# Performance work log

Hardware: AMD Instinct MI355X
Metric: run time of the kernel (lower is better)

## Reference

```python
import jax, jax.numpy as jnp
import numpy as np

INF = 1e5
EPS = 1e-8
B, NRES, NRIG = 1, 448, 512
C_S, C_Z, C_H, H, PQ, PV = 384, 128, 16, 12, 4, 8


def _quat_to_rot(q):
    q = q / jnp.linalg.norm(q, axis=-1, keepdims=True)
    w, x, y, z = q[..., 0], q[..., 1], q[..., 2], q[..., 3]
    return jnp.stack([
        jnp.stack([1 - 2 * (y * y + z * z), 2 * (x * y - w * z), 2 * (x * z + w * y)], -1),
        jnp.stack([2 * (x * y + w * z), 1 - 2 * (x * x + z * z), 2 * (y * z - w * x)], -1),
        jnp.stack([2 * (x * z - w * y), 2 * (y * z + w * x), 1 - 2 * (x * x + y * y)], -1),
    ], -2)


def setup_inputs() -> dict:
    key = jax.random.key(0)
    ks = jax.random.split(key, 16)
    lin = lambda k, i, o: (jax.random.normal(k, (i, o), jnp.float32) / np.sqrt(i))
    hc = H * C_H
    return dict(
        s=jax.random.normal(ks[0], (B, NRIG, C_S), jnp.float32),
        z=jax.random.normal(ks[1], (B, NRES, NRES, C_Z), jnp.float32),
        rot=_quat_to_rot(jax.random.normal(ks[2], (B, NRIG, 4), jnp.float32)),
        trans=jax.random.normal(ks[3], (B, NRIG, 3), jnp.float32) * 10.0,
        mask=jnp.ones((B, NRIG), jnp.float32),
        rigid_to_res_idx=jax.random.randint(ks[4], (B, NRIG), 0, NRES),
        w_q=lin(ks[5], C_S, hc), b_q=jnp.zeros((hc,), jnp.float32),
        w_kv=lin(ks[6], C_S, 2 * hc), b_kv=jnp.zeros((2 * hc,), jnp.float32),
        w_qp=lin(ks[7], C_S, H * PQ * 3), b_qp=jnp.zeros((H * PQ * 3,), jnp.float32),
        w_kvp=lin(ks[8], C_S, H * (PQ + PV) * 3), b_kvp=jnp.zeros((H * (PQ + PV) * 3,), jnp.float32),
        w_b=lin(ks[9], C_Z, H), b_b=jnp.zeros((H,), jnp.float32),
        w_dz=lin(ks[10], C_Z, C_Z // 4), b_dz=jnp.zeros((C_Z // 4,), jnp.float32),
        head_weights=jnp.full((H,), 0.5413, jnp.float32),  # softplus^-1(1)
        w_out=lin(ks[11], H * (C_Z // 4 + C_H + PV * 4), C_S),
        b_out=jnp.zeros((C_S,), jnp.float32),
    )


def _fwd(s, z, rot, trans, mask, rigid_to_res_idx,
         w_q, b_q, w_kv, b_kv, w_qp, b_qp, w_kvp, b_kvp,
         w_b, b_b, w_dz, b_dz, head_weights, w_out, b_out):
    Bd, nr, _ = s.shape
    nres = z.shape[-2]
    h = w_b.shape[-1]
    ch = w_q.shape[-1] // h
    pq = w_qp.shape[-1] // (3 * h)
    pkv = w_kvp.shape[-1] // (3 * h)
    pv = pkv - pq

    q = (s @ w_q + b_q).reshape(Bd, nr, h, ch)
    kv = (s @ w_kv + b_kv).reshape(Bd, nr, h, 2 * ch)
    k, v = kv[..., :ch], kv[..., ch:]

    def to_pts(flat):
        # flat: [B,nr,3*D] laid out as 3 coordinate chunks -> global-frame pts [B,nr,D,3]
        D = flat.shape[-1] // 3
        p = jnp.moveaxis(flat.reshape(Bd, nr, 3, D), -2, -1)
        return jnp.einsum('bnij,bndj->bndi', rot, p) + trans[:, :, None, :]

    q_pts = to_pts(s @ w_qp + b_qp).reshape(Bd, nr, h, pq, 3)
    kv_pts = to_pts(s @ w_kvp + b_kvp).reshape(Bd, nr, h, pkv, 3)
    k_pts, v_pts = kv_pts[..., :pq, :], kv_pts[..., pq:, :]

    # pair bias gathered rigid->res on both axes
    bi = jnp.arange(Bd)[:, None, None]
    b_pair = z @ w_b + b_b  # [B,Nres,Nres,H]
    b_bcast = b_pair[bi, rigid_to_res_idx[:, :, None], rigid_to_res_idx[:, None, :]]  # [B,nr,nr,H]

    a = jnp.einsum('bihc,bjhc->bhij', q, k) * np.sqrt(1.0 / (3 * ch))
    a = a + np.sqrt(1.0 / 3) * jnp.moveaxis(b_bcast, -1, -3)

    # squared-distance point attention
    diff = q_pts[:, :, None] - k_pts[:, None]  # [B,nr,nr,h,pq,3]
    sq = jnp.sum(diff * diff, -1)              # [B,nr,nr,h,pq]
    hw = jax.nn.softplus(head_weights) * np.sqrt(1.0 / (3 * (pq * 9.0 / 2)))
    pt_att = -0.5 * jnp.sum(sq * hw[:, None], -1)  # [B,nr,nr,h]
    a = a + jnp.moveaxis(pt_att, -1, -3)

    sq_mask = INF * (mask[:, :, None] * mask[:, None, :] - 1.0)
    a = jax.nn.softmax(a + sq_mask[:, None], axis=-1)  # [B,h,nr,nr]

    o = jnp.einsum('bhij,bjhc->bihc', a, v).reshape(Bd, nr, h * ch)

    o_pt_g = jnp.einsum('bhij,bjhpx->bihpx', a, v_pts)  # [B,nr,h,pv,3]
    o_pt = jnp.einsum('bnji,bnhpj->bnhpi', rot, o_pt_g - trans[:, :, None, None, :])  # invert_apply
    o_pt_norm = jnp.sqrt(jnp.sum(o_pt * o_pt, -1) + EPS).reshape(Bd, nr, h * pv)
    o_pt = o_pt.reshape(Bd, nr, h * pv, 3)

    pair_z = z @ w_dz + b_dz  # [B,Nres,Nres,cz4]
    pz_rig = pair_z[jnp.arange(Bd)[:, None], rigid_to_res_idx]  # [B,nr,Nres,cz4]
    # faithful to the torch scatter_add_: the index varies over the QUERY rigid i
    # (constant over keys j), so row i's full softmax mass lands in column res(i).
    onehot = jax.nn.one_hot(rigid_to_res_idx, nres, dtype=a.dtype)  # [B,nr,Nres]
    a_agg = a.sum(-1)[..., None] * onehot[:, None]  # [B,h,nr,Nres]
    o_pair = jnp.einsum('bhin,bind->bihd', a_agg, pz_rig).reshape(Bd, nr, -1)

    feats = jnp.concatenate([o, o_pt[..., 0], o_pt[..., 1], o_pt[..., 2], o_pt_norm, o_pair], -1)
    return feats @ w_out + b_out


def reference(s, z, rot, trans, mask, rigid_to_res_idx, w_q, b_q, w_kv, b_kv, w_qp, b_qp, w_kvp, b_kvp, w_b, b_b, w_dz, b_dz, head_weights, w_out, b_out):
    return _fwd(s, z, rot, trans, mask, rigid_to_res_idx, w_q, b_q, w_kv, b_kv, w_qp, b_qp, w_kvp, b_kvp, w_b, b_b, w_dz, b_dz, head_weights, w_out, b_out)
```

## Files before the change

### kernel.cpp

```cpp
#include <hip/hip_runtime.h>
#include <hip/hip_bf16.h>
#include <math.h>

constexpr int NRIG = 512;
constexpr int NRES = 448;
constexpr int CS   = 384;
constexpr int CZ   = 128;
constexpr int CH   = 16;
constexpr int NH   = 12;
constexpr int PQ   = 4;
constexpr int PV   = 8;
constexpr int HC   = NH * CH;
constexpr int NPAIR = NRES*NRES;
constexpr float INF_ = 100000.0f;
constexpr float SC_ = 0.57735026918962584f;

constexpr size_t OFF_Q   = 0;
constexpr size_t OFF_KT  = OFF_Q   + (size_t)NH*NRIG*16;
constexpr size_t OFF_QP  = OFF_KT  + (size_t)NH*16*NRIG;
constexpr size_t OFF_KPT = OFF_QP  + (size_t)NH*NRIG*12;
constexpr size_t OFF_VT  = OFF_KPT + (size_t)NH*12*NRIG;
constexpr size_t OFF_O   = OFF_VT  + (size_t)NH*40*NRIG;
constexpr size_t OFF_OPT = OFF_O   + (size_t)NRIG*HC;
constexpr size_t OFF_RS  = OFF_OPT + (size_t)NRIG*NH*PV*3;
constexpr size_t OFF_BP  = OFF_RS  + (size_t)NRIG*NH;
constexpr size_t OFF_RAW = OFF_BP  + (size_t)NH*NPAIR;
constexpr size_t OFF_F   = OFF_RAW + (size_t)NRIG*576;
constexpr size_t OFF_P3  = OFF_F   + (size_t)NRIG*960;

constexpr int ZWB_BLOCKS = NPAIR/128;

__global__ __launch_bounds__(256) void prep_kernel(
    const float* __restrict__ z,  const float* __restrict__ wb, const float* __restrict__ bb,
    const float* __restrict__ s,
    const float* __restrict__ wq,  const float* __restrict__ bq,
    const float* __restrict__ wkv, const float* __restrict__ bkv,
    const float* __restrict__ wqp, const float* __restrict__ bqp,
    const float* __restrict__ wkvp,const float* __restrict__ bkvp,
    float* __restrict__ ws)
{
    __shared__ float smem[3200];
    const int t = threadIdx.x;

    if ((int)blockIdx.x < ZWB_BLOCKS) {
        const int lane = t & 63;
        const int wid  = t >> 6;
        const int hh   = wid & 1;
        const int rgrp = wid >> 1;
        const int kbase = (lane & 7) * 16;
        const size_t r0 = (size_t)blockIdx.x * 128;

        float wv[16][6];
        #pragma unroll
        for (int kk = 0; kk < 16; ++kk)
            #pragma unroll
            for (int j = 0; j < 6; ++j)
                wv[kk][j] = wb[(size_t)(kbase + kk)*12 + hh*6 + j];

        float bbv[6];
        #pragma unroll
        for (int j = 0; j < 6; ++j) bbv[j] = bb[hh*6 + j];

        float* bp = ws + OFF_BP + (size_t)hh*6*NPAIR;

        for (int p = 0; p < 8; ++p) {
            const int oct = rgrp + 2*p;
            const size_t rowbase = r0 + (size_t)oct*8;
            const float4* zp = (const float4*)(z + (rowbase + (lane>>3))*CZ + kbase);

            float4 z0 = zp[0], z1 = zp[1], z2 = zp[2], z3 = zp[3];

            float acc[6] = {0.f,0.f,0.f,0.f,0.f,0.f};
            const float zr[16] = {z0.x,z0.y,z0.z,z0.w, z1.x,z1.y,z1.z,z1.w,
                                  z2.x,z2.y,z2.z,z2.w, z3.x,z3.y,z3.z,z3.w};
            #pragma unroll
            for (int kk = 0; kk < 16; ++kk) {
                const float zv = zr[kk];
                #pragma unroll
                for (int j = 0; j < 6; ++j) acc[j] += zv * wv[kk][j];
            }
            #pragma unroll
            for (int j = 0; j < 6; ++j) {
                acc[j] += __shfl_xor(acc[j], 1);
                acc[j] += __shfl_xor(acc[j], 2);
                acc[j] += __shfl_xor(acc[j], 4);
            }
            if ((lane & 7) == 0) {
                const size_t r = rowbase + (lane>>3);
                #pragma unroll
                for (int j = 0; j < 6; ++j)
                    bp[(size_t)j*NPAIR + r] = (acc[j] + bbv[j]) * SC_;
            }
        }
    } else {
        constexpr int BM=64, BN=32, BK=32, LDA=68;
        float (*sA)[LDA] = (float(*)[LDA])smem;
        float (*sB)[BN]  = (float(*)[BN])(smem + 2176);
        const int bid = (int)blockIdx.x - ZWB_BLOCKS;
        const int m0 = (bid & 7) * BM;
        const int c0 = (bid >> 3) * BN;
        const int tx = t & 15, ty = t >> 4;

        float acc[4][2] = {};
        for (int kt = 0; kt < CS/BK; ++kt) {
            const int k0 = kt*BK;
            #pragma unroll
            for (int r = 0; r < 2; ++r) {
                int qd = r*256 + t;
                int m = qd >> 3, kq = (qd & 7) << 2;
                float4 f = *(const float4*)(s + (size_t)(m0+m)*CS + k0 + kq);
                sA[kq+0][m] = f.x; sA[kq+1][m] = f.y;
                sA[kq+2][m] = f.z; sA[kq+3][m] = f.w;
            }
            {
                int kk = t >> 3, c4 = (t & 7) << 2;
                int c = c0 + c4;
                const float* wp; int ld, co;
                if (c < 192)      { wp = wq;   ld = 192; co = c;     }
                else if (c < 576) { wp = wkv;  ld = 384; co = c-192; }
                else if (c < 720) { wp = wqp;  ld = 144; co = c-576; }
                else              { wp = wkvp; ld = 432; co = c-720; }
                float4 f = *(const float4*)(wp + (size_t)(k0+kk)*ld + co);
                *(float4*)&sB[kk][c4] = f;
            }
            __syncthreads();
            #pragma unroll
            for (int kk = 0; kk < BK; ++kk) {
                float4 a = *(const float4*)&sA[kk][ty*4];
                float2 b = *(const float2*)&sB[kk][tx*2];
                acc[0][0] += a.x*b.x; acc[0][1] += a.x*b.y;
                acc[1][0] += a.y*b.x; acc[1][1] += a.y*b.y;
                acc[2][0] += a.z*b.x; acc[2][1] += a.z*b.y;
                acc[3][0] += a.w*b.x; acc[3][1] += a.w*b.y;
            }
            __syncthreads();
        }
        float* qw  = ws + OFF_Q;  float* ktw = ws + OFF_KT;  float* vt = ws + OFF_VT;
        float* raw = ws + OFF_RAW;
        #pragma unroll
        for (int i = 0; i < 4; ++i)
            #pragma unroll
            for (int j = 0; j < 2; ++j) {
                int n = m0 + ty*4 + i;
                int c = c0 + tx*2 + j;
                if (c < 192) {
                    int hh = c >> 4, cc = c & 15;
                    qw[((size_t)hh*NRIG + n)*16 + cc] = acc[i][j] + bq[c];
                } else if (c < 576) {
                    int e = c-192; float val = acc[i][j] + bkv[e];
                    int hh = e >> 5, sub = e & 31;
                    if (sub < CH) ktw[((size_t)hh*16 + sub)*NRIG + n] = val;
                    else          vt [((size_t)hh*40 + (sub-CH))*NRIG + n] = val;
                } else {
                    int e = c-576;
                    float bb_ = (c < 720) ? bqp[e] : bkvp[c-720];
                    raw[(size_t)n*576 + e] = acc[i][j] + bb_;
                }
            }
    }
}

__global__ __launch_bounds__(256) void rotate_kernel(
    const float* __restrict__ rot, const float* __restrict__ trans,
    const float* __restrict__ raw_in, float* __restrict__ qpw,
    float* __restrict__ kptw, float* __restrict__ vtw)
{
    const int gid = blockIdx.x*256 + threadIdx.x;
    const int n = gid / 192, d = gid % 192;
    const float* raw = raw_in + (size_t)n*576;
    float px, py, pzz;
    if (d < 48) { px = raw[d];      py = raw[48+d];       pzz = raw[96+d]; }
    else { int dd = d-48; px = raw[144+dd]; py = raw[288+dd]; pzz = raw[432+dd]; }
    const float* R = rot   + (size_t)n*9;
    const float* T = trans + (size_t)n*3;
    float gx = R[0]*px + R[1]*py + R[2]*pzz + T[0];
    float gy = R[3]*px + R[4]*py + R[5]*pzz + T[1];
    float gz = R[6]*px + R[7]*py + R[8]*pzz + T[2];
    if (d < 48) {
        int hh = d >> 2, pp = d & 3;
        float* dst = qpw + ((size_t)hh*NRIG + n)*12 + pp*3;
        dst[0]=gx; dst[1]=gy; dst[2]=gz;
    } else {
        int dd = d-48; int hh = dd/12, pp = dd%12;
        if (pp < PQ) {
            float* kpt = kptw + (size_t)hh*12*NRIG;
            kpt[(size_t)(pp*3+0)*NRIG + n] = gx;
            kpt[(size_t)(pp*3+1)*NRIG + n] = gy;
            kpt[(size_t)(pp*3+2)*NRIG + n] = gz;
        } else {
            float* vt = vtw + ((size_t)hh*40 + 16 + (pp-PQ)*3)*NRIG + n;
            vt[0*NRIG]=gx; vt[1*NRIG]=gy; vt[2*NRIG]=gz;
        }
    }
}

__global__ __launch_bounds__(256) void attn_kernel(
    const float* __restrict__ hw_in, const float* __restrict__ mask,
    const int* __restrict__ ridx,
    const float* __restrict__ qw_all,  const float* __restrict__ ktw_all,
    const float* __restrict__ qpw_all, const float* __restrict__ kpt_all,
    const float* __restrict__ vt_all,  const float* __restrict__ bp_all,
    float* __restrict__ o_out, float* __restrict__ opt_out, float* __restrict__ rs_out)
{
    constexpr int TI = 8;
    const int h    = blockIdx.x;
    const int i0   = blockIdx.y * TI;
    const int t    = threadIdx.x;
    const int lane = t & 63, wid = t >> 6;

    __shared__ float sE[TI*516];
    __shared__ float sP[16][TI][45];
    __shared__ float sS[TI];

    const float* qw  = qw_all  + (size_t)h*NRIG*16;
    const float* ktw = ktw_all + (size_t)h*16*NRIG;
    const float* qpw = qpw_all + (size_t)h*NRIG*12;
    const float* kpt = kpt_all + (size_t)h*12*NRIG;
    const float* vt  = vt_all  + (size_t)h*40*NRIG;
    const float* bph = bp_all  + (size_t)h*NPAIR;

    const float hwv = -0.5f * log1pf(__expf(hw_in[h])) * 0.13608276348795434f;
    const float QKS = 0.14433756729740643f;

    #pragma unroll
    for (int jj = 0; jj < 2; ++jj) {
        const int j = t + jj*256;
        float kk[16], kpv[12];
        #pragma unroll
        for (int c = 0; c < 16; ++c) kk[c]  = ktw[c*NRIG + j];
        #pragma unroll
        for (int e = 0; e < 12; ++e) kpv[e] = kpt[e*NRIG + j];
        const float mj = mask[j];
        const int   rj = ridx[j];
        #pragma unroll
        for (int qq = 0; qq < TI; ++qq) {
            const float* qv  = qw  + (size_t)(i0+qq)*16;
            const float* qpv = qpw + (size_t)(i0+qq)*12;
            const float  mi  = mask[i0+qq];
            const int    ri  = ridx[i0+qq];
            float dot = 0.f;
            #pragma unroll
            for (int c = 0; c < 16; ++c) dot += qv[c]*kk[c];
            float sq = 0.f;
            #pragma unroll
            for (int e = 0; e < 12; ++e) { float d = qpv[e]-kpv[e]; sq += d*d; }
            const float bv = bph[(size_t)ri*NRES + rj];
            const float lgt = dot*QKS + bv + hwv*sq + INF_*(mi*mj - 1.0f);
            sE[qq*516 + j] = __expf(lgt);
        }
    }
    __syncthreads();

    {
        float acc[11][TI];
        #pragma unroll
        for (int ci=0;ci<11;++ci)
            #pragma unroll
            for (int qq=0;qq<TI;++qq) acc[ci][qq]=0.f;

        #pragma unroll
        for (int m = 0; m < 8; ++m) {
            const int j = lane + (m<<6);
            float ev[TI];
            #pragma unroll
            for (int qq=0;qq<TI;++qq) ev[qq] = sE[qq*516 + j];
            #pragma unroll
            for (int ci = 0; ci < 11; ++ci) {
                if (ci < 10 || wid == 0) {
                    const int c = wid + (ci<<2);
                    const float vv = (c == 40) ? 1.0f : vt[(size_t)c*NRIG + j];
                    #pragma unroll
                    for (int qq=0;qq<TI;++qq) acc[ci][qq] += ev[qq]*vv;
                }
            }
        }
        #pragma unroll
        for (int ci=0;ci<11;++ci)
            if (ci < 10 || wid == 0)
                #pragma unroll
                for (int qq=0;qq<TI;++qq) {
                    acc[ci][qq] += __shfl_xor(acc[ci][qq], 1);
                    acc[ci][qq] += __shfl_xor(acc[ci][qq], 2);
                }
        if ((lane & 3) == 0) {
            const int g = lane >> 2;
            #pragma unroll
            for (int ci=0;ci<11;++ci)
                if (ci < 10 || wid == 0) {
                    const int c = wid + (ci<<2);
                    #pragma unroll
                    for (int qq=0;qq<TI;++qq) sP[g][qq][c] = acc[ci][qq];
                }
        }
    }
    __syncthreads();

    if (t < TI) {
        float S = 0.f;
        #pragma unroll
        for (int g = 0; g < 16; ++g) S += sP[g][t][40];
        sS[t] = S;
    }
    __syncthreads();

    for (int e = t; e < TI*41; e += 256) {
        const int qq = e / 41, c = e % 41;
        const int n = i0 + qq;
        float sum = 0.f;
        #pragma unroll
        for (int g = 0; g < 16; ++g) sum += sP[g][qq][c];
        const float val = sum * (1.0f / sS[qq]);
        if (c < 16)       o_out[((size_t)n*NH + h)*CH + c]        = val;
        else if (c < 40)  opt_out[((size_t)n*NH + h)*24 + (c-16)] = val;
        else              rs_out[(size_t)n*NH + h]                = val;
    }
}

__global__ __launch_bounds__(256) void feats_kernel(
    const float* __restrict__ rot, const float* __restrict__ trans,
    const float* __restrict__ z, const int* __restrict__ ridx,
    const float* __restrict__ wdz, const float* __restrict__ bdz,
    const float* __restrict__ o_ws, const float* __restrict__ optg,
    const float* __restrict__ rs, float* __restrict__ F)
{
    constexpr int TI = 4;
    __shared__ float sZd[TI][CZ];
    __shared__ float sPz[TI][32];
    const int i0 = blockIdx.x*TI;
    const int t  = threadIdx.x;

    for (int e = t; e < TI*CZ; e += 256) {
        int qq = e >> 7, c = e & 127;
        int ri = ridx[i0+qq];
        sZd[qq][c] = z[((size_t)ri*NRES + ri)*CZ + c];
    }
    for (int e = t; e < TI*HC; e += 256) {
        int qq = e/HC, c = e%HC;
        F[(size_t)(i0+qq)*960 + c] = o_ws[(size_t)(i0+qq)*HC + c];
    }
    for (int e = t; e < TI*96; e += 256) {
        int qq = e/96, hp = e%96; int n = i0+qq;
        const float* g = optg + ((size_t)n*NH + hp/PV)*24 + (hp%PV)*3;
        float gx = g[0]-trans[n*3+0], gy = g[1]-trans[n*3+1], gz = g[2]-trans[n*3+2];
        const float* R = rot + (size_t)n*9;
        float lx = R[0]*gx + R[3]*gy + R[6]*gz;
        float ly = R[1]*gx + R[4]*gy + R[7]*gz;
        float lz = R[2]*gx + R[5]*gy + R[8]*gz;
        float* Fr = F + (size_t)n*960;
        Fr[192+hp] = lx; Fr[288+hp] = ly; Fr[384+hp] = lz;
        Fr[480+hp] = sqrtf(lx*lx+ly*ly+lz*lz + 1e-8f);
    }
    __syncthreads();
    if (t < TI*32) {
        int qq = t >> 5, d = t & 31;
        float acc = 0.f;
        #pragma unroll 8
        for (int c = 0; c < CZ; ++c) acc += sZd[qq][c] * wdz[(size_t)c*32 + d];
        sPz[qq][d] = acc + bdz[d];
    }
    __syncthreads();
    for (int e = t; e < TI*384; e += 256) {
        int qq = e/384, hd = e%384; int n = i0+qq;
        F[(size_t)n*960 + 576 + hd] = rs[(size_t)n*NH + (hd>>5)] * sPz[qq][hd&31];
    }
}

__global__ __launch_bounds__(256) void out_gemm_kernel(
    const float* __restrict__ w_out, const float* __restrict__ F,
    float* __restrict__ P)
{
    constexpr int BM=64, BN=32, BK=32, LDA=68;
    __shared__ float sA[BK][LDA];
    __shared__ float sB[BK][BN];
    const int m0 = blockIdx.x * BM;
    const int c0 = blockIdx.y * BN;
    const int ks = blockIdx.z;
    const int t  = threadIdx.x;
    const int tx = t & 15, ty = t >> 4;

    float acc[4][2] = {};
    for (int kt = 0; kt < 10; ++kt) {
        const int k0 = ks*320 + kt*BK;
        #pragma unroll
        for (int r = 0; r < 2; ++r) {
            int qd = r*256 + t;
            int m = qd >> 3, kq = (qd & 7) << 2;
            float4 f = *(const float4*)(F + (size_t)(m0+m)*960 + k0 + kq);
            sA[kq+0][m] = f.x; sA[kq+1][m] = f.y;
            sA[kq+2][m] = f.z; sA[kq+3][m] = f.w;
        }
        {
            int kk = t >> 3, c4 = (t & 7) << 2;
            float4 f = *(const float4*)(w_out + (size_t)(k0+kk)*CS + c0 + c4);
            *(float4*)&sB[kk][c4] = f;
        }
        __syncthreads();
        #pragma unroll
        for (int kk = 0; kk < BK; ++kk) {
            float4 a = *(const float4*)&sA[kk][ty*4];
            float2 b = *(const float2*)&sB[kk][tx*2];
            acc[0][0] += a.x*b.x; acc[0][1] += a.x*b.y;
            acc[1][0] += a.y*b.x; acc[1][1] += a.y*b.y;
            acc[2][0] += a.z*b.x; acc[2][1] += a.z*b.y;
            acc[3][0] += a.w*b.x; acc[3][1] += a.w*b.y;
        }
        __syncthreads();
    }
    #pragma unroll
    for (int i = 0; i < 4; ++i)
        #pragma unroll
        for (int j = 0; j < 2; ++j) {
            int n = m0 + ty*4 + i;
            int c = c0 + tx*2 + j;
            P[(size_t)ks*NRIG*CS + (size_t)n*CS + c] = acc[i][j];
        }
}

__global__ __launch_bounds__(256) void reduce_kernel(
    const float* __restrict__ P, const float* __restrict__ b_out,
    float* __restrict__ out)
{
    const int i4 = blockIdx.x*256 + threadIdx.x;
    const size_t base = (size_t)i4 * 4;
    float4 a = *(const float4*)(P + base);
    float4 b = *(const float4*)(P + (size_t)NRIG*CS + base);
    float4 c = *(const float4*)(P + (size_t)2*NRIG*CS + base);
    const int cc = (int)(base % CS);
    float4 bv = *(const float4*)(b_out + cc);
    float4 r;
    r.x = a.x+b.x+c.x+bv.x; r.y = a.y+b.y+c.y+bv.y;
    r.z = a.z+b.z+c.z+bv.z; r.w = a.w+b.w+c.w+bv.w;
    *(float4*)(out + base) = r;
}

extern "C" void kernel_launch(void* const* d_in, const int* in_sizes, int n_in,
                              void* d_out, int out_size, void* d_ws, size_t ws_size,
                              hipStream_t stream)
{
    const float* s     = (const float*)d_in[0];
    const float* z     = (const float*)d_in[1];
    const float* rot   = (const float*)d_in[2];
    const float* trans = (const float*)d_in[3];
    const float* mask  = (const float*)d_in[4];
    const int*   ridx  = (const int*)  d_in[5];
    const float* wq    = (const float*)d_in[6];
    const float* bq    = (const float*)d_in[7];
    const float* wkv   = (const float*)d_in[8];
    const float* bkv   = (const float*)d_in[9];
    const float* wqp   = (const float*)d_in[10];
    const float* bqp   = (const float*)d_in[11];
    const float* wkvp  = (const float*)d_in[12];
    const float* bkvp  = (const float*)d_in[13];
    const float* wb    = (const float*)d_in[14];
    const float* bb    = (const float*)d_in[15];
    const float* wdz   = (const float*)d_in[16];
    const float* bdz   = (const float*)d_in[17];
    const float* hw    = (const float*)d_in[18];
    const float* wout  = (const float*)d_in[19];
    const float* bout  = (const float*)d_in[20];
    float* ws  = (float*)d_ws;
    float* out = (float*)d_out;

    hipLaunchKernelGGL(prep_kernel, dim3(ZWB_BLOCKS + 288), dim3(256), 0, stream,
        z, wb, bb, s, wq,bq, wkv,bkv, wqp,bqp, wkvp,bkvp, ws);
    hipLaunchKernelGGL(rotate_kernel, dim3(NRIG*192/256), dim3(256), 0, stream,
        rot, trans, ws+OFF_RAW, ws+OFF_QP, ws+OFF_KPT, ws+OFF_VT);
    hipLaunchKernelGGL(attn_kernel, dim3(NH, NRIG/8), dim3(256), 0, stream,
        hw, mask, ridx, ws+OFF_Q, ws+OFF_KT, ws+OFF_QP, ws+OFF_KPT,
        ws+OFF_VT, ws+OFF_BP, ws+OFF_O, ws+OFF_OPT, ws+OFF_RS);
    hipLaunchKernelGGL(feats_kernel, dim3(NRIG/4), dim3(256), 0, stream,
        rot, trans, z, ridx, wdz, bdz, ws+OFF_O, ws+OFF_OPT, ws+OFF_RS, ws+OFF_F);
    hipLaunchKernelGGL(out_gemm_kernel, dim3(NRIG/64, CS/32, 3), dim3(256), 0, stream,
        wout, ws+OFF_F, ws+OFF_P3);
    hipLaunchKernelGGL(reduce_kernel, dim3(NRIG*CS/4/256), dim3(256), 0, stream,
        ws+OFF_P3, bout, out);
}
```

Before: 126.8 us.

## Restructure z@w_b prep: 64-row blocks, 3 heads per wave, double-buffered z loads

The z-times-w_b bias projection now gives each block 64 rows, with each of the four waves covering 3 heads instead of 2 waves covering 6 heads each. The next 8-row z tile is prefetched into a second register set while the current one is computed. Launch bounds now request 4 blocks per SM. The intent is to hide global load latency, raise occupancy with fewer registers, and spread the bandwidth-bound z read over more blocks. The cost is that each z row is read by four waves instead of two, so more redundant loads, which L1/L2 must absorb.

```diff
diff --git a/kernel.cpp b/kernel.cpp
--- a/kernel.cpp
+++ b/kernel.cpp
@@ -28,9 +28,9 @@
 constexpr size_t OFF_F   = OFF_RAW + (size_t)NRIG*576;
 constexpr size_t OFF_P3  = OFF_F   + (size_t)NRIG*960;
 
-constexpr int ZWB_BLOCKS = NPAIR/128;
-
-__global__ __launch_bounds__(256) void prep_kernel(
+constexpr int ZWB_BLOCKS = NPAIR/64;
+
+__global__ __launch_bounds__(256, 4) void prep_kernel(
     const float* __restrict__ z,  const float* __restrict__ wb, const float* __restrict__ bb,
     const float* __restrict__ s,
     const float* __restrict__ wq,  const float* __restrict__ bq,
@@ -44,52 +44,55 @@
 
     if ((int)blockIdx.x < ZWB_BLOCKS) {
         const int lane = t & 63;
-        const int wid  = t >> 6;
-        const int hh   = wid & 1;
-        const int rgrp = wid >> 1;
-        const int kbase = (lane & 7) * 16;
-        const size_t r0 = (size_t)blockIdx.x * 128;
-
-        float wv[16][6];
-        #pragma unroll
-        for (int kk = 0; kk < 16; ++kk)
-            #pragma unroll
-            for (int j = 0; j < 6; ++j)
-                wv[kk][j] = wb[(size_t)(kbase + kk)*12 + hh*6 + j];
-
-        float bbv[6];
-        #pragma unroll
-        for (int j = 0; j < 6; ++j) bbv[j] = bb[hh*6 + j];
-
-        float* bp = ws + OFF_BP + (size_t)hh*6*NPAIR;
-
+        const int w    = t >> 6;
+        const int oct  = lane >> 3;
+        const int kl   = lane & 7;
+        const int kbase = kl << 4;
+        const size_t r0 = (size_t)blockIdx.x * 64;
+
+        float wv[16][3];
+        #pragma unroll
+        for (int kk = 0; kk < 16; ++kk) {
+            #pragma unroll
+            for (int j = 0; j < 3; ++j)
+                wv[kk][j] = wb[(size_t)(kbase + kk)*12 + 3*w + j];
+        }
+        const float bb0 = bb[3*w+0], bb1 = bb[3*w+1], bb2 = bb[3*w+2];
+        float* bp = ws + OFF_BP + (size_t)(3*w)*NPAIR;
+
+        float4 zbA0, zbA1, zbA2, zbA3;
+        float4 zbB0, zbB1, zbB2, zbB3;
+        {
+            const float4* zp = (const float4*)(z + (r0 + oct)*CZ + kbase);
+            zbA0 = zp[0]; zbA1 = zp[1]; zbA2 = zp[2]; zbA3 = zp[3];
+        }
+        #pragma unroll
         for (int p = 0; p < 8; ++p) {
-            const int oct = rgrp + 2*p;
-            const size_t rowbase = r0 + (size_t)oct*8;
-            const float4* zp = (const float4*)(z + (rowbase + (lane>>3))*CZ + kbase);
-
-            float4 z0 = zp[0], z1 = zp[1], z2 = zp[2], z3 = zp[3];
-
-            float acc[6] = {0.f,0.f,0.f,0.f,0.f,0.f};
-            const float zr[16] = {z0.x,z0.y,z0.z,z0.w, z1.x,z1.y,z1.z,z1.w,
-                                  z2.x,z2.y,z2.z,z2.w, z3.x,z3.y,z3.z,z3.w};
+            if (p < 7) {
+                const float4* zp = (const float4*)(z + (r0 + (size_t)(p+1)*8 + oct)*CZ + kbase);
+                if ((p & 1) == 0) { zbB0 = zp[0]; zbB1 = zp[1]; zbB2 = zp[2]; zbB3 = zp[3]; }
+                else              { zbA0 = zp[0]; zbA1 = zp[1]; zbA2 = zp[2]; zbA3 = zp[3]; }
+            }
+            const float4 c0 = ((p & 1) == 0) ? zbA0 : zbB0;
+            const float4 c1 = ((p & 1) == 0) ? zbA1 : zbB1;
+            const float4 c2 = ((p & 1) == 0) ? zbA2 : zbB2;
+            const float4 c3 = ((p & 1) == 0) ? zbA3 : zbB3;
+            const float zr[16] = {c0.x,c0.y,c0.z,c0.w, c1.x,c1.y,c1.z,c1.w,
+                                  c2.x,c2.y,c2.z,c2.w, c3.x,c3.y,c3.z,c3.w};
+            float a0 = 0.f, a1 = 0.f, a2 = 0.f;
             #pragma unroll
             for (int kk = 0; kk < 16; ++kk) {
                 const float zv = zr[kk];
-                #pragma unroll
-                for (int j = 0; j < 6; ++j) acc[j] += zv * wv[kk][j];
-            }
-            #pragma unroll
-            for (int j = 0; j < 6; ++j) {
-                acc[j] += __shfl_xor(acc[j], 1);
-                acc[j] += __shfl_xor(acc[j], 2);
-                acc[j] += __shfl_xor(acc[j], 4);
-            }
-            if ((lane & 7) == 0) {
-                const size_t r = rowbase + (lane>>3);
-                #pragma unroll
-                for (int j = 0; j < 6; ++j)
-                    bp[(size_t)j*NPAIR + r] = (acc[j] + bbv[j]) * SC_;
+                a0 += zv*wv[kk][0]; a1 += zv*wv[kk][1]; a2 += zv*wv[kk][2];
+            }
+            a0 += __shfl_xor(a0,1); a0 += __shfl_xor(a0,2); a0 += __shfl_xor(a0,4);
+            a1 += __shfl_xor(a1,1); a1 += __shfl_xor(a1,2); a1 += __shfl_xor(a1,4);
+            a2 += __shfl_xor(a2,1); a2 += __shfl_xor(a2,2); a2 += __shfl_xor(a2,4);
+            if (kl == 0) {
+                const size_t r = r0 + (size_t)p*8 + oct;
+                bp[r]                   = (a0 + bb0) * SC_;
+                bp[(size_t)NPAIR + r]   = (a1 + bb1) * SC_;
+                bp[(size_t)2*NPAIR + r] = (a2 + bb2) * SC_;
             }
         }
     } else {
```

Measured after the change: 130.2 us. 2.7% more time.
